# Performance work log

Hardware: AMD Instinct MI355X
Metric: run time of the kernel (lower is better)

The kernel has to match this reference:

```python
import jax, jax.numpy as jnp
import numpy as np

K = 3          # kernel_size
DILATION = 1
STRIDE = 1
B, C_IN, C_OUT, L = 16, 128, 128, 4096
L_OUT = L - DILATION * (K - 1)  # 'valid' padding, stride 1 -> 4094


def setup_inputs() -> dict:
    key = jax.random.key(0)
    k1, k2, k3, k4, k5 = jax.random.split(key, 5)
    x = jax.random.normal(k1, (B, C_IN, L), dtype=jnp.float32)
    offsets = jax.random.normal(k2, (B, 1, L_OUT, K), dtype=jnp.float32)
    mask = jax.random.uniform(k3, (B, K, L_OUT), dtype=jnp.float32)
    weight = jax.random.normal(k4, (C_OUT, C_IN, K), dtype=jnp.float32) * 0.05
    bias = jax.random.normal(k5, (C_OUT,), dtype=jnp.float32) * 0.05
    return {"x": x, "offsets": offsets, "mask": mask, "weight": weight, "bias": bias}


def _deform_conv1d(x, offsets, mask, weight, bias):
    b, c, l = x.shape
    l_out = offsets.shape[-2]
    dtype = offsets.dtype
    # dilated kernel positions: linspace(0, dil*K - dil, K) -> [0, 1, ..., K-1] for dil=1
    dil_pos = jnp.linspace(0.0, DILATION * K - DILATION, K, dtype=dtype)  # [K]
    t0s = (jnp.arange(l_out, dtype=dtype) * STRIDE)[:, None]             # [L_out, 1]
    T = t0s + dil_pos + offsets                                          # [B,1,L_out,K]
    # constrained sampling: keep each kernel's samples within its receptive field
    T = jnp.minimum(jnp.maximum(T, t0s), t0s + dil_pos[-1])
    U = jnp.clip(jnp.floor(T), 0, l - 2).astype(jnp.int32)               # [B,1,L_out,K] (detached)
    # gather left/right neighbors per channel
    idx = jnp.broadcast_to(U.reshape(b, 1, l_out * K), (b, c, l_out * K))
    x0 = jnp.take_along_axis(x, idx, axis=2).reshape(b, c, l_out, K)
    x1 = jnp.take_along_axis(x, idx + 1, axis=2).reshape(b, c, l_out, K)
    Uf = U.astype(dtype)
    G0 = jnp.maximum(0.0, 1.0 - jnp.abs(Uf - T))        # [B,1,L_out,K]
    G1 = jnp.maximum(0.0, 1.0 - jnp.abs(Uf + 1.0 - T))
    xs = G0 * x0 + G1 * x1                              # [B,C,L_out,K]
    # modulation mask: [B,K,L_out] -> [B,1,L_out,K]
    xs = xs * jnp.transpose(mask, (0, 2, 1))[:, None]
    # conv1d with stride == kernel_size over flattened [B,C,L_out*K] == per-position contraction
    out = jnp.einsum('bctk,ock->bot', xs, weight) + bias[None, :, None]
    return out  # [B, C_out, L_out]


def reference(x, offsets, mask, weight, bias):
    return _deform_conv1d(x, offsets, mask, weight, bias)
```

## Files before the change

kernel.cpp:

```cpp
#include <hip/hip_runtime.h>

#define BB 16
#define CI 128
#define CO 128
#define LL 4096
#define LOUT 4094
#define CK 384
#define TT 32
#define NTPB 4
#define STS 72
#define XSS 408

#define LDS_BARRIER() do { \
    asm volatile("s_waitcnt lgkmcnt(0)" ::: "memory"); \
    __builtin_amdgcn_s_barrier(); \
} while (0)

typedef short short8 __attribute__((ext_vector_type(8)));
typedef float floatx4 __attribute__((ext_vector_type(4)));

__device__ __forceinline__ ushort f2bf(float f) {
    union { float f; uint u; } v; v.f = f;
    uint r = v.u + 0x7FFFu + ((v.u >> 16) & 1u);
    return (ushort)(r >> 16);
}
__device__ __forceinline__ uint pk(ushort a, ushort b) {
    return (uint)a | ((uint)b << 16);
}
__device__ __forceinline__ short8 cvt8(floatx4 v0, floatx4 v1) {
    union { uint u[4]; short8 s; } r;
    r.u[0] = pk(f2bf(v0[0]), f2bf(v0[1]));
    r.u[1] = pk(f2bf(v0[2]), f2bf(v0[3]));
    r.u[2] = pk(f2bf(v1[0]), f2bf(v1[1]));
    r.u[3] = pk(f2bf(v1[2]), f2bf(v1[3]));
    return r.s;
}

__global__ __launch_bounds__(256)
void wcvt2_kernel(const float* __restrict__ w, ushort* __restrict__ wbf2) {
    const int i = blockIdx.x * 256 + threadIdx.x;
    const int o = i >> 7, c = i & 127;
    const float w0 = w[i * 3 + 0], w1 = w[i * 3 + 1], w2 = w[i * 3 + 2];
    wbf2[o * CK +       c] = f2bf(w0);
    wbf2[o * CK + 128 + c] = f2bf(w1);
    wbf2[o * CK + 256 + c] = f2bf(w2);
}

__global__ __launch_bounds__(512, 4)
void dconv1d_pers_kernel(const float* __restrict__ x,
                         const float* __restrict__ offs,
                         const float* __restrict__ mask,
                         const ushort* __restrict__ wbf2,
                         const float* __restrict__ bias,
                         float* __restrict__ out) {
    __shared__ ushort St[3][TT][STS];
    __shared__ ushort xs[TT][XSS];

    const int tid  = threadIdx.x;
    const int lane = tid & 63;
    const int wv   = tid >> 6;
    const int bid  = blockIdx.x;
    const int lb   = (bid & 7) * 64 + (bid >> 3);
    const int b    = lb >> 5;
    const int t0b  = (lb & 31) * (TT * NTPB);

    const int row16 = wv * 16 + (lane & 15);
    const int acol8 = (lane >> 4) << 3;

    short8 afr[12];
#pragma unroll
    for (int ks = 0; ks < 12; ++ks)
        afr[ks] = *(const short8*)(wbf2 + (size_t)row16 * CK + ks * 32 + acol8);

    const float* xrow = x + ((size_t)b * CI + row16) * LL;
    floatx4 c0a, c0b, c1a, c1b, xn0, xn1;
    {
        const int tb0 = t0b + acol8;
        const int tb1 = t0b + 32 + acol8;
        int tb2 = t0b + 64 + acol8; if (tb2 > LL - 8) tb2 = LL - 8;
        c0a = *(const floatx4*)(xrow + tb0); c0b = *(const floatx4*)(xrow + tb0 + 4);
        c1a = *(const floatx4*)(xrow + tb1); c1b = *(const floatx4*)(xrow + tb1 + 4);
        xn0 = *(const floatx4*)(xrow + tb2); xn1 = *(const floatx4*)(xrow + tb2 + 4);
    }

    const int ct  = tid & 31;
    const int ck_ = (tid >> 5) < 3 ? (tid >> 5) : 0;
    float ofc = 0.f, mvc = 0.f, ofn = 0.f, mvn = 0.f;
    if (tid < 96) {
        const int g0 = t0b + ct;
        ofc = offs[((size_t)b * LOUT + g0) * 3 + ck_];
        mvc = mask[((size_t)b * 3 + ck_) * LOUT + g0];
        const int g1 = t0b + TT + ct;
        if (g1 < LOUT) {
            ofn = offs[((size_t)b * LOUT + g1) * 3 + ck_];
            mvn = mask[((size_t)b * 3 + ck_) * LOUT + g1];
        }
    }

    float bv[4];
#pragma unroll
    for (int r = 0; r < 4; ++r)
        bv[r] = bias[wv * 16 + ((lane >> 4) << 2) + r];

    {
        uint* stz = (uint*)&St[0][0][0];
        for (int i = tid; i < 3 * TT * STS / 2; i += 512) stz[i] = 0;
    }

    short8 axf0 = cvt8(c0a, c0b);
    short8 axf1 = cvt8(c1a, c1b);
    LDS_BARRIER();

#pragma unroll 1
    for (int it = 0; it < NTPB; ++it) {
        const int t0 = t0b + it * TT;

        if (tid < 96) {
            const int gt = t0 + ct;
            float cc0 = 0.f, cc1 = 0.f, cc2 = 0.f, cc3 = 0.f;
            if (gt < LOUT) {
                const float gtf = (float)gt;
                float T = (gtf + (float)ck_) + ofc;
                T = fminf(fmaxf(T, gtf), gtf + 2.0f);
                int U = (int)floorf(T);
                if (U > LL - 2) U = LL - 2;
                const float Uf = (float)U;
                const float G0 = fmaxf(0.f, 1.f - fabsf(Uf - T)) * mvc;
                const float G1 = fmaxf(0.f, 1.f - fabsf(Uf + 1.f - T)) * mvc;
                const int d0 = U - gt;
                cc0 = (d0 == 0) ? G0 : 0.f;
                cc1 = (d0 == 0) ? G1 : ((d0 == 1) ? G0 : 0.f);
                cc2 = (d0 == 1) ? G1 : ((d0 == 2) ? G0 : 0.f);
                cc3 = (d0 == 2) ? G1 : 0.f;
            }
            St[ck_][ct][ct + 0] = f2bf(cc0);
            St[ck_][ct][ct + 1] = f2bf(cc1);
            St[ck_][ct][ct + 2] = f2bf(cc2);
            St[ck_][ct][ct + 3] = f2bf(cc3);
        }
        ofc = ofn; mvc = mvn;
        if (it + 2 < NTPB && tid < 96) {
            const int g = t0b + (it + 2) * TT + ct;
            ofn = 0.f; mvn = 0.f;
            if (g < LOUT) {
                ofn = offs[((size_t)b * LOUT + g) * 3 + ck_];
                mvn = mask[((size_t)b * 3 + ck_) * LOUT + g];
            }
        }
        LDS_BARRIER();

#pragma unroll
        for (int k = 0; k < 3; ++k) {
            floatx4 a1[2];
#pragma unroll
            for (int nf = 0; nf < 2; ++nf) {
                floatx4 z = {0.f, 0.f, 0.f, 0.f};
                a1[nf] = z;
            }
#pragma unroll
            for (int ks1 = 0; ks1 < 2; ++ks1) {
                const short8 a = ks1 ? axf1 : axf0;
                const short8 bfa = *(const short8*)
                    (&St[k][(lane & 15)][ks1 * 32 + acol8]);
                const short8 bfb = *(const short8*)
                    (&St[k][16 + (lane & 15)][ks1 * 32 + acol8]);
                a1[0] = __builtin_amdgcn_mfma_f32_16x16x32_bf16(a, bfa, a1[0], 0, 0, 0);
                a1[1] = __builtin_amdgcn_mfma_f32_16x16x32_bf16(a, bfb, a1[1], 0, 0, 0);
            }
#pragma unroll
            for (int nf = 0; nf < 2; ++nf) {
                const int tcol = nf * 16 + (lane & 15);
                const int cb   = wv * 16 + ((lane >> 4) << 2);
                uint2 q;
                q.x = pk(f2bf(a1[nf][0]), f2bf(a1[nf][1]));
                q.y = pk(f2bf(a1[nf][2]), f2bf(a1[nf][3]));
                *(uint2*)(&xs[tcol][k * 128 + cb]) = q;
            }
        }
        LDS_BARRIER();

        if (it + 1 < NTPB) {
            axf0 = axf1;
            axf1 = cvt8(xn0, xn1);
            if (it + 3 <= NTPB) {
                int tb = t0b + (it + 3) * 32 + acol8;
                if (tb > LL - 8) tb = LL - 8;
                xn0 = *(const floatx4*)(xrow + tb);
                xn1 = *(const floatx4*)(xrow + tb + 4);
            }
        }

        floatx4 acc[2];
#pragma unroll
        for (int nf = 0; nf < 2; ++nf) {
            floatx4 z = {0.f, 0.f, 0.f, 0.f};
            acc[nf] = z;
        }
#pragma unroll
        for (int ks = 0; ks < 12; ++ks) {
            const short8 bf0 = *(const short8*)(&xs[(lane & 15)][ks * 32 + acol8]);
            const short8 bf1 = *(const short8*)(&xs[16 + (lane & 15)][ks * 32 + acol8]);
            acc[0] = __builtin_amdgcn_mfma_f32_16x16x32_bf16(afr[ks], bf0, acc[0], 0, 0, 0);
            acc[1] = __builtin_amdgcn_mfma_f32_16x16x32_bf16(afr[ks], bf1, acc[1], 0, 0, 0);
        }

#pragma unroll
        for (int r = 0; r < 4; ++r) {
            const int o = wv * 16 + ((lane >> 4) << 2) + r;
            float* orow = out + ((size_t)b * CO + o) * LOUT;
#pragma unroll
            for (int nf = 0; nf < 2; ++nf) {
                const int gt = t0 + nf * 16 + (lane & 15);
                if (gt < LOUT) orow[gt] = acc[nf][r] + bv[r];
            }
        }
    }
}

extern "C" void kernel_launch(void* const* d_in, const int* in_sizes, int n_in,
                              void* d_out, int out_size, void* d_ws, size_t ws_size,
                              hipStream_t stream) {
    const float* x    = (const float*)d_in[0];
    const float* offs = (const float*)d_in[1];
    const float* mask = (const float*)d_in[2];
    const float* w    = (const float*)d_in[3];
    const float* bias = (const float*)d_in[4];
    float* out = (float*)d_out;
    ushort* wbf2 = (ushort*)d_ws;

    wcvt2_kernel<<<dim3(CO * CI / 256), dim3(256), 0, stream>>>(w, wbf2);
    dconv1d_pers_kernel<<<dim3(512), dim3(512), 0, stream>>>(
        x, offs, mask, wbf2, bias, out);
}
```

Before: 33.95 us.

## Give each wave two 16-row M fragments and halve block size

Each wave now owns 32 output and input-channel rows as two MFMA M fragments instead of 16 rows. Every B fragment read from LDS (St and xs) then feeds two MFMAs, which cuts LDS read traffic per MFMA. The block shrinks from 8 to 4 waves, and the launch bound becomes 256 threads with 2 blocks. In exchange, registers per thread roughly double for weight fragments and accumulators, and fewer waves are resident to hide global-memory latency.

New measurement: 33.75 us. No clear change (-0.6%).

```diff
diff --git a/kernel.cpp b/kernel.cpp
--- a/kernel.cpp
+++ b/kernel.cpp
@@ -46,13 +46,13 @@
     wbf2[o * CK + 256 + c] = f2bf(w2);
 }
 
-__global__ __launch_bounds__(512, 4)
-void dconv1d_pers_kernel(const float* __restrict__ x,
-                         const float* __restrict__ offs,
-                         const float* __restrict__ mask,
-                         const ushort* __restrict__ wbf2,
-                         const float* __restrict__ bias,
-                         float* __restrict__ out) {
+__global__ __launch_bounds__(256, 2)
+void dconv1d_mf2_kernel(const float* __restrict__ x,
+                        const float* __restrict__ offs,
+                        const float* __restrict__ mask,
+                        const ushort* __restrict__ wbf2,
+                        const float* __restrict__ bias,
+                        float* __restrict__ out) {
     __shared__ ushort St[3][TT][STS];
     __shared__ ushort xs[TT][XSS];
 
@@ -64,23 +64,30 @@
     const int b    = lb >> 5;
     const int t0b  = (lb & 31) * (TT * NTPB);
 
-    const int row16 = wv * 16 + (lane & 15);
+    const int r15   = lane & 15;
     const int acol8 = (lane >> 4) << 3;
 
-    short8 afr[12];
+    short8 afr[12][2];
 #pragma unroll
     for (int ks = 0; ks < 12; ++ks)
-        afr[ks] = *(const short8*)(wbf2 + (size_t)row16 * CK + ks * 32 + acol8);
-
-    const float* xrow = x + ((size_t)b * CI + row16) * LL;
-    floatx4 c0a, c0b, c1a, c1b, xn0, xn1;
+#pragma unroll
+        for (int mf = 0; mf < 2; ++mf)
+            afr[ks][mf] = *(const short8*)
+                (wbf2 + (size_t)(wv * 32 + mf * 16 + r15) * CK + ks * 32 + acol8);
+
+    const float* xrow0 = x + ((size_t)b * CI + wv * 32 +      r15) * LL;
+    const float* xrow1 = x + ((size_t)b * CI + wv * 32 + 16 + r15) * LL;
+    floatx4 c0[2][2], c1[2][2], xn[2][2];
     {
         const int tb0 = t0b + acol8;
         const int tb1 = t0b + 32 + acol8;
-        int tb2 = t0b + 64 + acol8; if (tb2 > LL - 8) tb2 = LL - 8;
-        c0a = *(const floatx4*)(xrow + tb0); c0b = *(const floatx4*)(xrow + tb0 + 4);
-        c1a = *(const floatx4*)(xrow + tb1); c1b = *(const floatx4*)(xrow + tb1 + 4);
-        xn0 = *(const floatx4*)(xrow + tb2); xn1 = *(const floatx4*)(xrow + tb2 + 4);
+        const int tb2 = t0b + 64 + acol8;
+        c0[0][0] = *(const floatx4*)(xrow0 + tb0); c0[0][1] = *(const floatx4*)(xrow0 + tb0 + 4);
+        c0[1][0] = *(const floatx4*)(xrow1 + tb0); c0[1][1] = *(const floatx4*)(xrow1 + tb0 + 4);
+        c1[0][0] = *(const floatx4*)(xrow0 + tb1); c1[0][1] = *(const floatx4*)(xrow0 + tb1 + 4);
+        c1[1][0] = *(const floatx4*)(xrow1 + tb1); c1[1][1] = *(const floatx4*)(xrow1 + tb1 + 4);
+        xn[0][0] = *(const floatx4*)(xrow0 + tb2); xn[0][1] = *(const floatx4*)(xrow0 + tb2 + 4);
+        xn[1][0] = *(const floatx4*)(xrow1 + tb2); xn[1][1] = *(const floatx4*)(xrow1 + tb2 + 4);
     }
 
     const int ct  = tid & 31;
@@ -97,18 +104,24 @@
         }
     }
 
-    float bv[4];
-#pragma unroll
-    for (int r = 0; r < 4; ++r)
-        bv[r] = bias[wv * 16 + ((lane >> 4) << 2) + r];
+    float bv[2][4];
+#pragma unroll
+    for (int mf = 0; mf < 2; ++mf)
+#pragma unroll
+        for (int r = 0; r < 4; ++r)
+            bv[mf][r] = bias[wv * 32 + mf * 16 + ((lane >> 4) << 2) + r];
 
     {
         uint* stz = (uint*)&St[0][0][0];
-        for (int i = tid; i < 3 * TT * STS / 2; i += 512) stz[i] = 0;
-    }
-
-    short8 axf0 = cvt8(c0a, c0b);
-    short8 axf1 = cvt8(c1a, c1b);
+        for (int i = tid; i < 3 * TT * STS / 2; i += 256) stz[i] = 0;
+    }
+
+    short8 axf[2][2];
+#pragma unroll
+    for (int mf = 0; mf < 2; ++mf) {
+        axf[mf][0] = cvt8(c0[mf][0], c0[mf][1]);
+        axf[mf][1] = cvt8(c1[mf][0], c1[mf][1]);
+    }
     LDS_BARRIER();
 
 #pragma unroll 1
@@ -151,69 +164,85 @@
 
 #pragma unroll
         for (int k = 0; k < 3; ++k) {
-            floatx4 a1[2];
-#pragma unroll
-            for (int nf = 0; nf < 2; ++nf) {
-                floatx4 z = {0.f, 0.f, 0.f, 0.f};
-                a1[nf] = z;
-            }
+            floatx4 a1[2][2];
+#pragma unroll
+            for (int mf = 0; mf < 2; ++mf)
+#pragma unroll
+                for (int nf = 0; nf < 2; ++nf) {
+                    floatx4 z = {0.f, 0.f, 0.f, 0.f};
+                    a1[mf][nf] = z;
+                }
 #pragma unroll
             for (int ks1 = 0; ks1 < 2; ++ks1) {
-                const short8 a = ks1 ? axf1 : axf0;
-                const short8 bfa = *(const short8*)
-                    (&St[k][(lane & 15)][ks1 * 32 + acol8]);
-                const short8 bfb = *(const short8*)
-                    (&St[k][16 + (lane & 15)][ks1 * 32 + acol8]);
-                a1[0] = __builtin_amdgcn_mfma_f32_16x16x32_bf16(a, bfa, a1[0], 0, 0, 0);
-                a1[1] = __builtin_amdgcn_mfma_f32_16x16x32_bf16(a, bfb, a1[1], 0, 0, 0);
-            }
-#pragma unroll
-            for (int nf = 0; nf < 2; ++nf) {
-                const int tcol = nf * 16 + (lane & 15);
-                const int cb   = wv * 16 + ((lane >> 4) << 2);
-                uint2 q;
-                q.x = pk(f2bf(a1[nf][0]), f2bf(a1[nf][1]));
-                q.y = pk(f2bf(a1[nf][2]), f2bf(a1[nf][3]));
-                *(uint2*)(&xs[tcol][k * 128 + cb]) = q;
-            }
+                const short8 bfa = *(const short8*)(&St[k][r15][ks1 * 32 + acol8]);
+                const short8 bfb = *(const short8*)(&St[k][16 + r15][ks1 * 32 + acol8]);
+#pragma unroll
+                for (int mf = 0; mf < 2; ++mf) {
+                    a1[mf][0] = __builtin_amdgcn_mfma_f32_16x16x32_bf16(axf[mf][ks1], bfa, a1[mf][0], 0, 0, 0);
+                    a1[mf][1] = __builtin_amdgcn_mfma_f32_16x16x32_bf16(axf[mf][ks1], bfb, a1[mf][1], 0, 0, 0);
+                }
+            }
+#pragma unroll
+            for (int mf = 0; mf < 2; ++mf)
+#pragma unroll
+                for (int nf = 0; nf < 2; ++nf) {
+                    const int tcol = nf * 16 + r15;
+                    const int cb   = wv * 32 + mf * 16 + ((lane >> 4) << 2);
+                    uint2 q;
+                    q.x = pk(f2bf(a1[mf][nf][0]), f2bf(a1[mf][nf][1]));
+                    q.y = pk(f2bf(a1[mf][nf][2]), f2bf(a1[mf][nf][3]));
+                    *(uint2*)(&xs[tcol][k * 128 + cb]) = q;
+                }
         }
         LDS_BARRIER();
 
         if (it + 1 < NTPB) {
-            axf0 = axf1;
-            axf1 = cvt8(xn0, xn1);
+#pragma unroll
+            for (int mf = 0; mf < 2; ++mf) {
+                axf[mf][0] = axf[mf][1];
+                axf[mf][1] = cvt8(xn[mf][0], xn[mf][1]);
+            }
             if (it + 3 <= NTPB) {
                 int tb = t0b + (it + 3) * 32 + acol8;
                 if (tb > LL - 8) tb = LL - 8;
-                xn0 = *(const floatx4*)(xrow + tb);
-                xn1 = *(const floatx4*)(xrow + tb + 4);
-            }
-        }
-
-        floatx4 acc[2];
-#pragma unroll
-        for (int nf = 0; nf < 2; ++nf) {
-            floatx4 z = {0.f, 0.f, 0.f, 0.f};
-            acc[nf] = z;
-        }
+                xn[0][0] = *(const floatx4*)(xrow0 + tb);
+                xn[0][1] = *(const floatx4*)(xrow0 + tb + 4);
+                xn[1][0] = *(const floatx4*)(xrow1 + tb);
+                xn[1][1] = *(const floatx4*)(xrow1 + tb + 4);
+            }
+        }
+
+        floatx4 acc[2][2];
+#pragma unroll
+        for (int mf = 0; mf < 2; ++mf)
+#pragma unroll
+            for (int nf = 0; nf < 2; ++nf) {
+                floatx4 z = {0.f, 0.f, 0.f, 0.f};
+                acc[mf][nf] = z;
+            }
 #pragma unroll
         for (int ks = 0; ks < 12; ++ks) {
-            const short8 bf0 = *(const short8*)(&xs[(lane & 15)][ks * 32 + acol8]);
-            const short8 bf1 = *(const short8*)(&xs[16 + (lane & 15)][ks * 32 + acol8]);
-            acc[0] = __builtin_amdgcn_mfma_f32_16x16x32_bf16(afr[ks], bf0, acc[0], 0, 0, 0);
-            acc[1] = __builtin_amdgcn_mfma_f32_16x16x32_bf16(afr[ks], bf1, acc[1], 0, 0, 0);
-        }
-
-#pragma unroll
-        for (int r = 0; r < 4; ++r) {
-            const int o = wv * 16 + ((lane >> 4) << 2) + r;
-            float* orow = out + ((size_t)b * CO + o) * LOUT;
-#pragma unroll
-            for (int nf = 0; nf < 2; ++nf) {
-                const int gt = t0 + nf * 16 + (lane & 15);
-                if (gt < LOUT) orow[gt] = acc[nf][r] + bv[r];
-            }
-        }
+            const short8 bf0 = *(const short8*)(&xs[r15][ks * 32 + acol8]);
+            const short8 bf1 = *(const short8*)(&xs[16 + r15][ks * 32 + acol8]);
+#pragma unroll
+            for (int mf = 0; mf < 2; ++mf) {
+                acc[mf][0] = __builtin_amdgcn_mfma_f32_16x16x32_bf16(afr[ks][mf], bf0, acc[mf][0], 0, 0, 0);
+                acc[mf][1] = __builtin_amdgcn_mfma_f32_16x16x32_bf16(afr[ks][mf], bf1, acc[mf][1], 0, 0, 0);
+            }
+        }
+
+#pragma unroll
+        for (int mf = 0; mf < 2; ++mf)
+#pragma unroll
+            for (int r = 0; r < 4; ++r) {
+                const int o = wv * 32 + mf * 16 + ((lane >> 4) << 2) + r;
+                float* orow = out + ((size_t)b * CO + o) * LOUT;
+#pragma unroll
+                for (int nf = 0; nf < 2; ++nf) {
+                    const int gt = t0 + nf * 16 + r15;
+                    if (gt < LOUT) orow[gt] = acc[mf][nf][r] + bv[mf][r];
+                }
+            }
     }
 }
 
@@ -229,6 +258,6 @@
     ushort* wbf2 = (ushort*)d_ws;
 
     wcvt2_kernel<<<dim3(CO * CI / 256), dim3(256), 0, stream>>>(w, wbf2);
-    dconv1d_pers_kernel<<<dim3(512), dim3(512), 0, stream>>>(
+    dconv1d_mf2_kernel<<<dim3(512), dim3(256), 0, stream>>>(
         x, offs, mask, wbf2, bias, out);
 }
```
